# Performance work log

Hardware: AMD Instinct MI355X
Metric: run time of the kernel (lower is better)

## Reference

```python
import jax, jax.numpy as jnp
import numpy as np

N_NODES = 25000
N_EDGES = 800000
NUM_GRAPHS = 512
EMB = 128
OUT_EMB = 256
NUM_RADIAL = 6
NUM_DENSE = 3
NUM_TARGETS = 12


def setup_inputs() -> dict:
    key = jax.random.key(0)
    ks = jax.random.split(key, 10)
    m = jax.random.normal(ks[0], (N_EDGES, EMB), dtype=jnp.float32)
    rbf = jax.random.normal(ks[1], (N_EDGES, NUM_RADIAL), dtype=jnp.float32)
    edge_src = jax.random.randint(ks[2], (N_EDGES,), 0, N_NODES, dtype=jnp.int32)
    node2graph = jnp.sort(jax.random.randint(ks[3], (N_NODES,), 0, NUM_GRAPHS, dtype=jnp.int32))
    w_rbf = jax.random.normal(ks[4], (NUM_RADIAL, EMB), dtype=jnp.float32) * 0.4
    w_up = jax.random.normal(ks[5], (EMB, OUT_EMB), dtype=jnp.float32) * 0.08
    w_dense = jax.random.normal(ks[6], (NUM_DENSE, OUT_EMB, OUT_EMB), dtype=jnp.float32) * 0.06
    b_dense = jax.random.normal(ks[7], (NUM_DENSE, OUT_EMB), dtype=jnp.float32) * 0.01
    w_final = jax.random.normal(ks[8], (OUT_EMB, NUM_TARGETS), dtype=jnp.float32) * 0.05
    return {"m": m, "rbf": rbf, "edge_src": edge_src, "node2graph": node2graph,
            "w_rbf": w_rbf, "w_up": w_up, "w_dense": w_dense, "b_dense": b_dense,
            "w_final": w_final, "num_graphs": NUM_GRAPHS}


def reference(m, rbf, edge_src, node2graph, w_rbf, w_up, w_dense, b_dense, w_final, num_graphs):
    n_nodes = node2graph.shape[0]
    # edge: tmp = m * dense_rbf(rbf)   [E, emb]
    tmp = m * (rbf @ w_rbf)
    # reverse graph + copy_e/sum == scatter-sum per-edge tmp into original src node
    t = jax.ops.segment_sum(tmp, edge_src, num_segments=n_nodes)  # [N, emb]
    # up projection (no bias)
    t = t @ w_up  # [N, out_emb]
    # dense layers with swish activation
    for i in range(w_dense.shape[0]):
        t = jax.nn.silu(t @ w_dense[i] + b_dense[i])
    # final projection (no bias)
    t = t @ w_final  # [N, num_targets]
    # extensive readout: per-graph sum over nodes
    return jax.ops.segment_sum(t, node2graph, num_segments=num_graphs)  # [G, num_targets]
```

## Files before the change

### kernel.cpp

```cpp
#include <hip/hip_runtime.h>
#include <hip/hip_bf16.h>
#include <math.h>

#define EMB 128
#define OUT 256
#define RAD 6
#define NDL 3
#define NTGT 12
#define MT 32
#define S 264
#define ECH 1024

typedef __attribute__((ext_vector_type(8))) short short8;
typedef __attribute__((ext_vector_type(4))) float floatx4;

__device__ inline short f2bf(float x) {
    __hip_bfloat16 h = __float2bfloat16(x);
    return *reinterpret_cast<short*>(&h);
}


__global__ void hist_kernel(const int* __restrict__ src, int* __restrict__ counts, int E) {
    int i = blockIdx.x * blockDim.x + threadIdx.x;
    if (i < E) atomicAdd(&counts[src[i]], 1);
}

__global__ void scan_kernel(const int* __restrict__ counts, int* __restrict__ offs,
                            int* __restrict__ cursor, int N) {
    __shared__ int sums[1024];
    int tid = threadIdx.x;
    int chunk = (N + 1023) / 1024;
    int beg = tid * chunk;
    int end = min(beg + chunk, N);
    int s = 0;
    for (int i = beg; i < end; i++) s += counts[i];
    int mysum = s;
    sums[tid] = s;
    __syncthreads();
    for (int off = 1; off < 1024; off <<= 1) {
        int add = (tid >= off) ? sums[tid - off] : 0;
        __syncthreads();
        sums[tid] += add;
        __syncthreads();
    }
    int prefix = sums[tid] - mysum;
    for (int i = beg; i < end; i++) {
        int c = counts[i];
        offs[i] = prefix;
        cursor[i] = prefix;
        prefix += c;
    }
    if (tid == 0) offs[N] = sums[1023];
}

__global__ void scatter_kernel(const int* __restrict__ src, int* __restrict__ cursor,
                               int* __restrict__ eids, int E) {
    int i = blockIdx.x * blockDim.x + threadIdx.x;
    if (i < E) {
        int pos = atomicAdd(&cursor[src[i]], 1);
        eids[pos] = i;
    }
}


__global__ void prep_kernel(const float* __restrict__ w_up, const float* __restrict__ w_dense,
                            const float* __restrict__ w_final,
                            short* __restrict__ w_upT, short* __restrict__ w_dT,
                            short* __restrict__ w_fT) {
    const int T1 = OUT * EMB;
    const int T2 = NDL * OUT * OUT;
    const int T3 = 16 * OUT;
    int total = T1 + T2 + T3;
    for (int i = blockIdx.x * blockDim.x + threadIdx.x; i < total; i += gridDim.x * blockDim.x) {
        if (i < T1) {
            int n = i >> 7, k = i & 127;
            w_upT[i] = f2bf(w_up[k * OUT + n]);
        } else if (i < T1 + T2) {
            int j = i - T1;
            int l = j >> 16, o = (j >> 8) & 255, k = j & 255;
            w_dT[j] = f2bf(w_dense[(l << 16) + (k << 8) + o]);
        } else {
            int j = i - T1 - T2;
            int t = j >> 8, k = j & 255;
            w_fT[j] = (t < NTGT) ? f2bf(w_final[k * NTGT + t]) : (short)0;
        }
    }
}


__global__ __launch_bounds__(128) void gather_kernel(
    const float* __restrict__ m, const float* __restrict__ rbf,
    const float* __restrict__ w_rbf,
    const int* __restrict__ offs, const int* __restrict__ eids,
    __hip_bfloat16* __restrict__ t0, int N) {

    __shared__ int sEid[ECH];
    __shared__ float sRed[32 * 4];

    int n = blockIdx.x;
    int tid = threadIdx.x;
    int grp = tid >> 5;
    int c = tid & 31;

    float4 wq[RAD];
#pragma unroll
    for (int r = 0; r < RAD; r++) wq[r] = *(const float4*)&w_rbf[r * EMB + 4 * c];

    int b = offs[n], e = offs[n + 1];
    float ax = 0.f, ay = 0.f, az = 0.f, aw = 0.f;

    for (int base = b; base < e; base += ECH) {
        int cnt = min(ECH, e - base);
        __syncthreads();
        for (int i = tid; i < cnt; i += 128) sEid[i] = eids[base + i];
        __syncthreads();

        int i = grp;
        for (; i + 8 <= cnt; i += 8) {
            int e0 = sEid[i], e1 = sEid[i + 4];
            const float* rb0 = &rbf[(size_t)e0 * RAD];
            const float* rb1 = &rbf[(size_t)e1 * RAD];
            float2 p0 = *(const float2*)&rb0[0];
            float2 p1 = *(const float2*)&rb0[2];
            float2 p2 = *(const float2*)&rb0[4];
            float2 q0 = *(const float2*)&rb1[0];
            float2 q1 = *(const float2*)&rb1[2];
            float2 q2 = *(const float2*)&rb1[4];
            float4 m0 = *(const float4*)&m[(size_t)e0 * EMB + 4 * c];
            float4 m1 = *(const float4*)&m[(size_t)e1 * EMB + 4 * c];

            float cx0 = wq[0].x * p0.x + wq[1].x * p0.y + wq[2].x * p1.x + wq[3].x * p1.y + wq[4].x * p2.x + wq[5].x * p2.y;
            float cy0 = wq[0].y * p0.x + wq[1].y * p0.y + wq[2].y * p1.x + wq[3].y * p1.y + wq[4].y * p2.x + wq[5].y * p2.y;
            float cz0 = wq[0].z * p0.x + wq[1].z * p0.y + wq[2].z * p1.x + wq[3].z * p1.y + wq[4].z * p2.x + wq[5].z * p2.y;
            float cw0 = wq[0].w * p0.x + wq[1].w * p0.y + wq[2].w * p1.x + wq[3].w * p1.y + wq[4].w * p2.x + wq[5].w * p2.y;
            ax += m0.x * cx0; ay += m0.y * cy0; az += m0.z * cz0; aw += m0.w * cw0;

            float cx1 = wq[0].x * q0.x + wq[1].x * q0.y + wq[2].x * q1.x + wq[3].x * q1.y + wq[4].x * q2.x + wq[5].x * q2.y;
            float cy1 = wq[0].y * q0.x + wq[1].y * q0.y + wq[2].y * q1.x + wq[3].y * q1.y + wq[4].y * q2.x + wq[5].y * q2.y;
            float cz1 = wq[0].z * q0.x + wq[1].z * q0.y + wq[2].z * q1.x + wq[3].z * q1.y + wq[4].z * q2.x + wq[5].z * q2.y;
            float cw1 = wq[0].w * q0.x + wq[1].w * q0.y + wq[2].w * q1.x + wq[3].w * q1.y + wq[4].w * q2.x + wq[5].w * q2.y;
            ax += m1.x * cx1; ay += m1.y * cy1; az += m1.z * cz1; aw += m1.w * cw1;
        }
        for (; i < cnt; i += 4) {
            int e0 = sEid[i];
            const float* rb0 = &rbf[(size_t)e0 * RAD];
            float2 p0 = *(const float2*)&rb0[0];
            float2 p1 = *(const float2*)&rb0[2];
            float2 p2 = *(const float2*)&rb0[4];
            float4 m0 = *(const float4*)&m[(size_t)e0 * EMB + 4 * c];
            float cx0 = wq[0].x * p0.x + wq[1].x * p0.y + wq[2].x * p1.x + wq[3].x * p1.y + wq[4].x * p2.x + wq[5].x * p2.y;
            float cy0 = wq[0].y * p0.x + wq[1].y * p0.y + wq[2].y * p1.x + wq[3].y * p1.y + wq[4].y * p2.x + wq[5].y * p2.y;
            float cz0 = wq[0].z * p0.x + wq[1].z * p0.y + wq[2].z * p1.x + wq[3].z * p1.y + wq[4].z * p2.x + wq[5].z * p2.y;
            float cw0 = wq[0].w * p0.x + wq[1].w * p0.y + wq[2].w * p1.x + wq[3].w * p1.y + wq[4].w * p2.x + wq[5].w * p2.y;
            ax += m0.x * cx0; ay += m0.y * cy0; az += m0.z * cz0; aw += m0.w * cw0;
        }
    }

    ax += __shfl_xor(ax, 32); ay += __shfl_xor(ay, 32);
    az += __shfl_xor(az, 32); aw += __shfl_xor(aw, 32);
    __syncthreads();
    if (tid >= 64 && tid < 96) {
        sRed[c * 4 + 0] = ax; sRed[c * 4 + 1] = ay;
        sRed[c * 4 + 2] = az; sRed[c * 4 + 3] = aw;
    }
    __syncthreads();
    if (tid < 32) {
        ax += sRed[c * 4 + 0]; ay += sRed[c * 4 + 1];
        az += sRed[c * 4 + 2]; aw += sRed[c * 4 + 3];
        __hip_bfloat16* dst = t0 + (size_t)n * EMB + 4 * c;
        dst[0] = __float2bfloat16(ax);
        dst[1] = __float2bfloat16(ay);
        dst[2] = __float2bfloat16(az);
        dst[3] = __float2bfloat16(aw);
    }
}


__global__ __launch_bounds__(256) void chain_kernel(
    const __hip_bfloat16* __restrict__ t0,
    const short* __restrict__ w_upT, const short* __restrict__ w_dT,
    const float* __restrict__ b_dense, const short* __restrict__ w_fT,
    const int* __restrict__ node2graph, float* __restrict__ out, int N) {

    __shared__ short sA[2][MT * S];

    int tid = threadIdx.x;
    int n0 = blockIdx.x * MT;
    int wave = tid >> 6, lane = tid & 63;
    int lo = lane & 15;
    int quad = lane >> 4;
    int kq = quad * 8;
    int wcol = wave * 64;

    {
        int r = tid >> 3;
        int c = (tid & 7) * 16;
        uint4 v0 = {0, 0, 0, 0}, v1 = {0, 0, 0, 0};
        if (n0 + r < N) {
            const uint4* src = (const uint4*)((const short*)t0 + (size_t)(n0 + r) * EMB + c);
            v0 = src[0];
            v1 = src[1];
        }
        *(uint4*)&sA[0][r * S + c] = v0;
        *(uint4*)&sA[0][r * S + c + 8] = v1;
    }
    __syncthreads();

    auto layer = [&](int cur, int K, const short* __restrict__ Bt,
                     const float* __restrict__ bias, bool act) {
        floatx4 acc[2][4];
#pragma unroll
        for (int mt = 0; mt < 2; mt++)
#pragma unroll
            for (int nt = 0; nt < 4; nt++)
                acc[mt][nt] = floatx4{0.f, 0.f, 0.f, 0.f};

        for (int kc = 0; kc < K; kc += 32) {
            short8 a0 = *(const short8*)&sA[cur][(lo) * S + kc + kq];
            short8 a1 = *(const short8*)&sA[cur][(16 + lo) * S + kc + kq];
#pragma unroll
            for (int nt = 0; nt < 4; nt++) {
                int n = wcol + nt * 16 + lo;
                short8 b = *(const short8*)&Bt[(size_t)n * K + kc + kq];
                acc[0][nt] = __builtin_amdgcn_mfma_f32_16x16x32_bf16(a0, b, acc[0][nt], 0, 0, 0);
                acc[1][nt] = __builtin_amdgcn_mfma_f32_16x16x32_bf16(a1, b, acc[1][nt], 0, 0, 0);
            }
        }

        float bv[4];
#pragma unroll
        for (int nt = 0; nt < 4; nt++) bv[nt] = bias ? bias[wcol + nt * 16 + lo] : 0.f;

        short* dst = sA[cur ^ 1];
#pragma unroll
        for (int mt = 0; mt < 2; mt++)
#pragma unroll
            for (int nt = 0; nt < 4; nt++) {
                int n = wcol + nt * 16 + lo;
#pragma unroll
                for (int i = 0; i < 4; i++) {
                    int mrow = mt * 16 + quad * 4 + i;
                    float x = acc[mt][nt][i] + bv[nt];
                    if (act) x = x / (1.f + __expf(-x));
                    dst[mrow * S + n] = f2bf(x);
                }
            }
        __syncthreads();
    };

    layer(0, EMB, w_upT, nullptr, false);
    layer(1, OUT, w_dT + 0 * OUT * OUT, b_dense + 0 * OUT, true);
    layer(0, OUT, w_dT + 1 * OUT * OUT, b_dense + 1 * OUT, true);
    layer(1, OUT, w_dT + 2 * OUT * OUT, b_dense + 2 * OUT, true);

    if (wave == 0) {
        floatx4 facc[2];
        facc[0] = floatx4{0.f, 0.f, 0.f, 0.f};
        facc[1] = floatx4{0.f, 0.f, 0.f, 0.f};
        for (int kc = 0; kc < OUT; kc += 32) {
            short8 a0 = *(const short8*)&sA[0][(lo) * S + kc + kq];
            short8 a1 = *(const short8*)&sA[0][(16 + lo) * S + kc + kq];
            short8 b = *(const short8*)&w_fT[lo * OUT + kc + kq];
            facc[0] = __builtin_amdgcn_mfma_f32_16x16x32_bf16(a0, b, facc[0], 0, 0, 0);
            facc[1] = __builtin_amdgcn_mfma_f32_16x16x32_bf16(a1, b, facc[1], 0, 0, 0);
        }
        if (lo < NTGT) {
#pragma unroll
            for (int mt = 0; mt < 2; mt++)
#pragma unroll
                for (int i = 0; i < 4; i++) {
                    int node = n0 + mt * 16 + quad * 4 + i;
                    if (node < N)
                        atomicAdd(&out[node2graph[node] * NTGT + lo], facc[mt][i]);
                }
        }
    }
}


extern "C" void kernel_launch(void* const* d_in, const int* in_sizes, int n_in,
                              void* d_out, int out_size, void* d_ws, size_t ws_size,
                              hipStream_t stream) {
    const float* m        = (const float*)d_in[0];
    const float* rbf      = (const float*)d_in[1];
    const int*   edge_src = (const int*)d_in[2];
    const int*   node2g   = (const int*)d_in[3];
    const float* w_rbf    = (const float*)d_in[4];
    const float* w_up     = (const float*)d_in[5];
    const float* w_dense  = (const float*)d_in[6];
    const float* b_dense  = (const float*)d_in[7];
    const float* w_final  = (const float*)d_in[8];

    int E = in_sizes[2];
    int N = in_sizes[3];
    float* out = (float*)d_out;

    char* p = (char*)d_ws;
    auto alloc = [&](size_t bytes) {
        char* r = p;
        p += (bytes + 255) & ~(size_t)255;
        return r;
    };
    int*   counts = (int*)alloc((size_t)N * 4);
    int*   offs   = (int*)alloc((size_t)(N + 1) * 4);
    int*   cursor = (int*)alloc((size_t)N * 4);
    int*   eids   = (int*)alloc((size_t)E * 4);
    __hip_bfloat16* t0 = (__hip_bfloat16*)alloc((size_t)N * EMB * 2);
    short* w_upT  = (short*)alloc((size_t)OUT * EMB * 2);
    short* w_dT   = (short*)alloc((size_t)NDL * OUT * OUT * 2);
    short* w_fT   = (short*)alloc((size_t)16 * OUT * 2);

    hipMemsetAsync(counts, 0, (size_t)N * 4, stream);
    hipMemsetAsync(d_out, 0, (size_t)out_size * 4, stream);

    prep_kernel<<<512, 256, 0, stream>>>(w_up, w_dense, w_final, w_upT, w_dT, w_fT);
    hist_kernel<<<(E + 255) / 256, 256, 0, stream>>>(edge_src, counts, E);
    scan_kernel<<<1, 1024, 0, stream>>>(counts, offs, cursor, N);
    scatter_kernel<<<(E + 255) / 256, 256, 0, stream>>>(edge_src, cursor, eids, E);
    gather_kernel<<<N, 128, 0, stream>>>(m, rbf, w_rbf, offs, eids, t0, N);
    chain_kernel<<<(N + MT - 1) / MT, 256, 0, stream>>>(t0, w_upT, w_dT, b_dense,
                                                        w_fT, node2g, out, N);
}
```

Measured before the change: 763.3 us.

## Fuse edge gather-reduce into MLP chain kernel, one wave per node row

```diff
diff --git a/kernel.cpp b/kernel.cpp
--- a/kernel.cpp
+++ b/kernel.cpp
@@ -9,7 +9,6 @@
 #define NTGT 12
 #define MT 32
 #define S 264
-#define ECH 1024
 
 typedef __attribute__((ext_vector_type(8))) short short8;
 typedef __attribute__((ext_vector_type(4))) float floatx4;
@@ -17,6 +16,12 @@
 __device__ inline short f2bf(float x) {
     __hip_bfloat16 h = __float2bfloat16(x);
     return *reinterpret_cast<short*>(&h);
+}
+
+__device__ inline unsigned pack2bf(float x, float y) {
+    unsigned a = (unsigned short)f2bf(x);
+    unsigned b = (unsigned short)f2bf(y);
+    return a | (b << 16);
 }
 
 
@@ -88,121 +93,78 @@
 }
 
 
-__global__ __launch_bounds__(128) void gather_kernel(
+__global__ __launch_bounds__(256) void fused_kernel(
     const float* __restrict__ m, const float* __restrict__ rbf,
     const float* __restrict__ w_rbf,
     const int* __restrict__ offs, const int* __restrict__ eids,
-    __hip_bfloat16* __restrict__ t0, int N) {
-
-    __shared__ int sEid[ECH];
-    __shared__ float sRed[32 * 4];
-
-    int n = blockIdx.x;
-    int tid = threadIdx.x;
-    int grp = tid >> 5;
-    int c = tid & 31;
-
-    float4 wq[RAD];
-#pragma unroll
-    for (int r = 0; r < RAD; r++) wq[r] = *(const float4*)&w_rbf[r * EMB + 4 * c];
-
-    int b = offs[n], e = offs[n + 1];
-    float ax = 0.f, ay = 0.f, az = 0.f, aw = 0.f;
-
-    for (int base = b; base < e; base += ECH) {
-        int cnt = min(ECH, e - base);
-        __syncthreads();
-        for (int i = tid; i < cnt; i += 128) sEid[i] = eids[base + i];
-        __syncthreads();
-
-        int i = grp;
-        for (; i + 8 <= cnt; i += 8) {
-            int e0 = sEid[i], e1 = sEid[i + 4];
-            const float* rb0 = &rbf[(size_t)e0 * RAD];
-            const float* rb1 = &rbf[(size_t)e1 * RAD];
-            float2 p0 = *(const float2*)&rb0[0];
-            float2 p1 = *(const float2*)&rb0[2];
-            float2 p2 = *(const float2*)&rb0[4];
-            float2 q0 = *(const float2*)&rb1[0];
-            float2 q1 = *(const float2*)&rb1[2];
-            float2 q2 = *(const float2*)&rb1[4];
-            float4 m0 = *(const float4*)&m[(size_t)e0 * EMB + 4 * c];
-            float4 m1 = *(const float4*)&m[(size_t)e1 * EMB + 4 * c];
-
-            float cx0 = wq[0].x * p0.x + wq[1].x * p0.y + wq[2].x * p1.x + wq[3].x * p1.y + wq[4].x * p2.x + wq[5].x * p2.y;
-            float cy0 = wq[0].y * p0.x + wq[1].y * p0.y + wq[2].y * p1.x + wq[3].y * p1.y + wq[4].y * p2.x + wq[5].y * p2.y;
-            float cz0 = wq[0].z * p0.x + wq[1].z * p0.y + wq[2].z * p1.x + wq[3].z * p1.y + wq[4].z * p2.x + wq[5].z * p2.y;
-            float cw0 = wq[0].w * p0.x + wq[1].w * p0.y + wq[2].w * p1.x + wq[3].w * p1.y + wq[4].w * p2.x + wq[5].w * p2.y;
-            ax += m0.x * cx0; ay += m0.y * cy0; az += m0.z * cz0; aw += m0.w * cw0;
-
-            float cx1 = wq[0].x * q0.x + wq[1].x * q0.y + wq[2].x * q1.x + wq[3].x * q1.y + wq[4].x * q2.x + wq[5].x * q2.y;
-            float cy1 = wq[0].y * q0.x + wq[1].y * q0.y + wq[2].y * q1.x + wq[3].y * q1.y + wq[4].y * q2.x + wq[5].y * q2.y;
-            float cz1 = wq[0].z * q0.x + wq[1].z * q0.y + wq[2].z * q1.x + wq[3].z * q1.y + wq[4].z * q2.x + wq[5].z * q2.y;
-            float cw1 = wq[0].w * q0.x + wq[1].w * q0.y + wq[2].w * q1.x + wq[3].w * q1.y + wq[4].w * q2.x + wq[5].w * q2.y;
-            ax += m1.x * cx1; ay += m1.y * cy1; az += m1.z * cz1; aw += m1.w * cw1;
-        }
-        for (; i < cnt; i += 4) {
-            int e0 = sEid[i];
-            const float* rb0 = &rbf[(size_t)e0 * RAD];
-            float2 p0 = *(const float2*)&rb0[0];
-            float2 p1 = *(const float2*)&rb0[2];
-            float2 p2 = *(const float2*)&rb0[4];
-            float4 m0 = *(const float4*)&m[(size_t)e0 * EMB + 4 * c];
-            float cx0 = wq[0].x * p0.x + wq[1].x * p0.y + wq[2].x * p1.x + wq[3].x * p1.y + wq[4].x * p2.x + wq[5].x * p2.y;
-            float cy0 = wq[0].y * p0.x + wq[1].y * p0.y + wq[2].y * p1.x + wq[3].y * p1.y + wq[4].y * p2.x + wq[5].y * p2.y;
-            float cz0 = wq[0].z * p0.x + wq[1].z * p0.y + wq[2].z * p1.x + wq[3].z * p1.y + wq[4].z * p2.x + wq[5].z * p2.y;
-            float cw0 = wq[0].w * p0.x + wq[1].w * p0.y + wq[2].w * p1.x + wq[3].w * p1.y + wq[4].w * p2.x + wq[5].w * p2.y;
-            ax += m0.x * cx0; ay += m0.y * cy0; az += m0.z * cz0; aw += m0.w * cw0;
-        }
-    }
-
-    ax += __shfl_xor(ax, 32); ay += __shfl_xor(ay, 32);
-    az += __shfl_xor(az, 32); aw += __shfl_xor(aw, 32);
-    __syncthreads();
-    if (tid >= 64 && tid < 96) {
-        sRed[c * 4 + 0] = ax; sRed[c * 4 + 1] = ay;
-        sRed[c * 4 + 2] = az; sRed[c * 4 + 3] = aw;
-    }
-    __syncthreads();
-    if (tid < 32) {
-        ax += sRed[c * 4 + 0]; ay += sRed[c * 4 + 1];
-        az += sRed[c * 4 + 2]; aw += sRed[c * 4 + 3];
-        __hip_bfloat16* dst = t0 + (size_t)n * EMB + 4 * c;
-        dst[0] = __float2bfloat16(ax);
-        dst[1] = __float2bfloat16(ay);
-        dst[2] = __float2bfloat16(az);
-        dst[3] = __float2bfloat16(aw);
-    }
-}
-
-
-__global__ __launch_bounds__(256) void chain_kernel(
-    const __hip_bfloat16* __restrict__ t0,
     const short* __restrict__ w_upT, const short* __restrict__ w_dT,
     const float* __restrict__ b_dense, const short* __restrict__ w_fT,
     const int* __restrict__ node2graph, float* __restrict__ out, int N) {
 
     __shared__ short sA[2][MT * S];
 
-    int tid = threadIdx.x;
-    int n0 = blockIdx.x * MT;
-    int wave = tid >> 6, lane = tid & 63;
-    int lo = lane & 15;
-    int quad = lane >> 4;
-    int kq = quad * 8;
-    int wcol = wave * 64;
-
-    {
-        int r = tid >> 3;
-        int c = (tid & 7) * 16;
-        uint4 v0 = {0, 0, 0, 0}, v1 = {0, 0, 0, 0};
-        if (n0 + r < N) {
-            const uint4* src = (const uint4*)((const short*)t0 + (size_t)(n0 + r) * EMB + c);
-            v0 = src[0];
-            v1 = src[1];
-        }
-        *(uint4*)&sA[0][r * S + c] = v0;
-        *(uint4*)&sA[0][r * S + c + 8] = v1;
+    const int tid = threadIdx.x;
+    const int n0 = blockIdx.x * MT;
+    const int wave = tid >> 6, lane = tid & 63;
+    const int lo = lane & 15;
+    const int quad = lane >> 4;
+    const int kq = quad * 8;
+    const int wcol = wave * 64;
+
+    float2 wq[RAD];
+#pragma unroll
+    for (int r = 0; r < RAD; r++) wq[r] = *(const float2*)&w_rbf[r * EMB + 2 * lane];
+
+#pragma unroll 1
+    for (int s = 0; s < 8; s++) {
+        const int r = wave * 8 + s;
+        const int n = n0 + r;
+        float ax = 0.f, ay = 0.f;
+        if (n < N) {
+            const int b = offs[n], e = offs[n + 1];
+            int i = b;
+            for (; i + 4 <= e; i += 4) {
+                int ev[4];
+                float2 mv[4];
+                float2 rv[4][3];
+#pragma unroll
+                for (int j = 0; j < 4; j++) ev[j] = eids[i + j];
+#pragma unroll
+                for (int j = 0; j < 4; j++) {
+                    const float* rb = &rbf[(size_t)ev[j] * RAD];
+                    rv[j][0] = *(const float2*)&rb[0];
+                    rv[j][1] = *(const float2*)&rb[2];
+                    rv[j][2] = *(const float2*)&rb[4];
+                    mv[j] = *(const float2*)&m[(size_t)ev[j] * EMB + 2 * lane];
+                }
+#pragma unroll
+                for (int j = 0; j < 4; j++) {
+                    float cx = wq[0].x * rv[j][0].x + wq[1].x * rv[j][0].y
+                             + wq[2].x * rv[j][1].x + wq[3].x * rv[j][1].y
+                             + wq[4].x * rv[j][2].x + wq[5].x * rv[j][2].y;
+                    float cy = wq[0].y * rv[j][0].x + wq[1].y * rv[j][0].y
+                             + wq[2].y * rv[j][1].x + wq[3].y * rv[j][1].y
+                             + wq[4].y * rv[j][2].x + wq[5].y * rv[j][2].y;
+                    ax += mv[j].x * cx;
+                    ay += mv[j].y * cy;
+                }
+            }
+            for (; i < e; i++) {
+                int e0 = eids[i];
+                const float* rb = &rbf[(size_t)e0 * RAD];
+                float2 p0 = *(const float2*)&rb[0];
+                float2 p1 = *(const float2*)&rb[2];
+                float2 p2 = *(const float2*)&rb[4];
+                float2 m0 = *(const float2*)&m[(size_t)e0 * EMB + 2 * lane];
+                float cx = wq[0].x * p0.x + wq[1].x * p0.y + wq[2].x * p1.x
+                         + wq[3].x * p1.y + wq[4].x * p2.x + wq[5].x * p2.y;
+                float cy = wq[0].y * p0.x + wq[1].y * p0.y + wq[2].y * p1.x
+                         + wq[3].y * p1.y + wq[4].y * p2.x + wq[5].y * p2.y;
+                ax += m0.x * cx;
+                ay += m0.y * cy;
+            }
+        }
+        *(unsigned*)&sA[0][r * S + 2 * lane] = pack2bf(ax, ay);
     }
     __syncthreads();
 
@@ -305,7 +267,6 @@
     int*   offs   = (int*)alloc((size_t)(N + 1) * 4);
     int*   cursor = (int*)alloc((size_t)N * 4);
     int*   eids   = (int*)alloc((size_t)E * 4);
-    __hip_bfloat16* t0 = (__hip_bfloat16*)alloc((size_t)N * EMB * 2);
     short* w_upT  = (short*)alloc((size_t)OUT * EMB * 2);
     short* w_dT   = (short*)alloc((size_t)NDL * OUT * OUT * 2);
     short* w_fT   = (short*)alloc((size_t)16 * OUT * 2);
@@ -317,7 +278,7 @@
     hist_kernel<<<(E + 255) / 256, 256, 0, stream>>>(edge_src, counts, E);
     scan_kernel<<<1, 1024, 0, stream>>>(counts, offs, cursor, N);
     scatter_kernel<<<(E + 255) / 256, 256, 0, stream>>>(edge_src, cursor, eids, E);
-    gather_kernel<<<N, 128, 0, stream>>>(m, rbf, w_rbf, offs, eids, t0, N);
-    chain_kernel<<<(N + MT - 1) / MT, 256, 0, stream>>>(t0, w_upT, w_dT, b_dense,
-                                                        w_fT, node2g, out, N);
-}
+    fused_kernel<<<(N + MT - 1) / MT, 256, 0, stream>>>(m, rbf, w_rbf, offs, eids,
+                                                        w_upT, w_dT, b_dense, w_fT,
+                                                        node2g, out, N);
+}
```

New measurement: 811.7 us. 6.3% more time.
